# Performance work log

Measured on AMD Instinct MI355X. Metric: run time of the kernel, lower is better.

Reference implementation:

```python
import jax, jax.numpy as jnp
import numpy as np

TEMPERATURE = 0.07
NEG_INF = -9e15
EPS = 1e-12

def setup_inputs() -> dict:
    key = jax.random.key(0)
    k1, k2 = jax.random.split(key)
    N, D = 8192, 128
    features = jax.random.normal(k1, (N, D), dtype=jnp.float32)
    labels = jax.random.randint(k2, (N,), 0, 16, dtype=jnp.int64)
    return {"features": features, "labels": labels}

def reference(features, labels):
    N = features.shape[0]
    # L2 normalize rows (torch F.normalize: x / max(||x||, eps))
    norm = jnp.linalg.norm(features, axis=1, keepdims=True)
    f = features / jnp.maximum(norm, EPS)
    # [N, N] similarity
    sim = jnp.matmul(f, f.T) / TEMPERATURE
    eye = jnp.eye(N, dtype=bool)
    sim = jnp.where(eye, NEG_INF, sim)
    # positive-pair mask: same label, excluding self
    pos_mask = ((labels[:, None] == labels[None, :]) & ~eye).astype(sim.dtype)
    denom = jnp.exp(sim).sum(axis=1, keepdims=True)  # [N, 1]
    log_prob = sim - jnp.log(denom + EPS)
    loss = -(pos_mask * log_prob).sum(axis=1) / (pos_mask.sum(axis=1) + EPS)
    return loss.mean()
```

## Files before the change

### kernel.cpp

```cpp
#include <hip/hip_runtime.h>
#include <hip/hip_bf16.h>

#define EPS 1e-12f
#define SQRT_C_EXP 4.53981597f
#define M_LN2F 0.69314718056f
#define NUM_CLASSES 16
#define CS_BLOCKS 128

#define BM 256
#define BN 128
#define KD 128
#define NCHUNK 8
#define NPART 16

typedef __attribute__((ext_vector_type(4))) float f32x4;
typedef __attribute__((ext_vector_type(8))) short bf16x8;

__device__ __forceinline__ float bf2f(ushort u) {
    unsigned int x = ((unsigned int)u) << 16;
    return __uint_as_float(x);
}

__device__ __forceinline__ const bf16x8* lds_frag(const ushort* base, int r, int slot) {
    int sw = slot ^ (r & 7);
    return reinterpret_cast<const bf16x8*>(
        reinterpret_cast<const char*>(base) + r * 256 + sw * 16);
}

__global__ void normalize_kernel(const float* __restrict__ feat,
                                 ushort* __restrict__ fb,
                                 float* __restrict__ sq,
                                 float* __restrict__ gz,
                                 int N) {
    if (blockIdx.x == 0) {
        for (int i = threadIdx.x; i < NUM_CLASSES * KD + NUM_CLASSES; i += 256)
            gz[i] = 0.f;
    }
    int r    = (blockIdx.x * blockDim.x + threadIdx.x) >> 6;
    int lane = threadIdx.x & 63;
    if (r >= N) return;
    const float2 v = *reinterpret_cast<const float2*>(feat + (size_t)r * KD + lane * 2);
    float s = v.x * v.x + v.y * v.y;
    #pragma unroll
    for (int off = 1; off < 64; off <<= 1) s += __shfl_xor(s, off);
    const float scale = SQRT_C_EXP / fmaxf(sqrtf(s), EPS);

    __hip_bfloat16 h0 = __float2bfloat16(v.x * scale);
    __hip_bfloat16 h1 = __float2bfloat16(v.y * scale);
    ushort u0 = *reinterpret_cast<ushort*>(&h0);
    ushort u1 = *reinterpret_cast<ushort*>(&h1);
    unsigned int pack = (unsigned int)u0 | ((unsigned int)u1 << 16);
    *reinterpret_cast<unsigned int*>(fb + (size_t)r * KD + lane * 2) = pack;

    float q0 = bf2f(u0), q1 = bf2f(u1);
    float q = q0 * q0 + q1 * q1;
    #pragma unroll
    for (int off = 1; off < 64; off <<= 1) q += __shfl_xor(q, off);
    if (lane == 0) sq[r] = q;
}

__global__ __launch_bounds__(256) void classsum_kernel(
    const ushort* __restrict__ fb,
    const int* __restrict__ labels,
    float* __restrict__ g,
    float* __restrict__ cntf,
    int N) {
    __shared__ float lds[2][NUM_CLASSES][128];
    __shared__ float ldc[2][NUM_CLASSES];
    const int d    = threadIdx.x & 127;
    const int half = threadIdx.x >> 7;
    #pragma unroll
    for (int c = 0; c < NUM_CLASSES; c++) lds[half][c][d] = 0.f;
    if (d < NUM_CLASSES) ldc[half][d] = 0.f;
    __syncthreads();

    const int r0 = blockIdx.x * 64 + half * 32;
    for (int r = r0; r < r0 + 32; r++) {
        int lab = labels[r];
        lds[half][lab][d] += bf2f(fb[(size_t)r * KD + d]);
        if (d == 0) ldc[half][lab] += 1.f;
    }
    __syncthreads();

    for (int c = half; c < NUM_CLASSES; c += 2)
        atomicAdd(&g[c * KD + d], lds[0][c][d] + lds[1][c][d]);
    if (threadIdx.x < NUM_CLASSES)
        atomicAdd(&cntf[threadIdx.x], ldc[0][threadIdx.x] + ldc[1][threadIdx.x]);
}

__global__ __launch_bounds__(512, 2) void supcon_denom(
    const ushort* __restrict__ fb,
    float* __restrict__ denom_part,
    int N) {

    __shared__ __align__(16) ushort As[BM * KD];
    __shared__ __align__(16) ushort Bs[2][BN * KD];

    const int tid  = threadIdx.x;
    const int lane = tid & 63;
    const int w    = tid >> 6;
    const int wr   = w >> 1;
    const int wc   = w & 1;
    const int r16  = lane & 15;
    const int g4   = lane >> 4;

    const int rowbase = blockIdx.y * BM;
    const int col0    = blockIdx.x * (BN * NCHUNK);

    {
        const ushort* gA = fb + (size_t)rowbase * KD;
        #pragma unroll
        for (int i = 0; i < 8; i++) {
            int c = i * 512 + tid;
            bf16x8 v = *reinterpret_cast<const bf16x8*>(gA + c * 8);
            int dst = c ^ ((c >> 4) & 7);
            *reinterpret_cast<bf16x8*>(&As[dst * 8]) = v;
        }
        const ushort* gB = fb + (size_t)col0 * KD;
        #pragma unroll
        for (int i = 0; i < 4; i++) {
            int c = i * 512 + tid;
            bf16x8 v = *reinterpret_cast<const bf16x8*>(gB + c * 8);
            int dst = c ^ ((c >> 4) & 7);
            *reinterpret_cast<bf16x8*>(&Bs[0][dst * 8]) = v;
        }
    }
    __syncthreads();

    bf16x8 a[4][4];
    #pragma unroll
    for (int ks = 0; ks < 4; ks++) {
        const int slot = ks * 4 + g4;
        #pragma unroll
        for (int m = 0; m < 4; m++)
            a[ks][m] = *lds_frag(As, wr * 64 + m * 16 + r16, slot);
    }

    float pd[4][4];
    #pragma unroll
    for (int m = 0; m < 4; m++)
        #pragma unroll
        for (int i = 0; i < 4; i++) pd[m][i] = 0.f;

    int cur = 0;
    for (int c = 0; c < NCHUNK; c++) {
        bf16x8 pre0, pre1, pre2, pre3;
        if (c + 1 < NCHUNK) {
            const ushort* gB = fb + (size_t)(col0 + (c + 1) * BN) * KD;
            pre0 = *reinterpret_cast<const bf16x8*>(gB + (0 * 512 + tid) * 8);
            pre1 = *reinterpret_cast<const bf16x8*>(gB + (1 * 512 + tid) * 8);
            pre2 = *reinterpret_cast<const bf16x8*>(gB + (2 * 512 + tid) * 8);
            pre3 = *reinterpret_cast<const bf16x8*>(gB + (3 * 512 + tid) * 8);
        }

        f32x4 acc[4][4];
        #pragma unroll
        for (int m = 0; m < 4; m++)
            #pragma unroll
            for (int n = 0; n < 4; n++) acc[m][n] = f32x4{0.f, 0.f, 0.f, 0.f};

        const ushort* bbase = Bs[cur];
        #pragma unroll
        for (int ks = 0; ks < 4; ks++) {
            const int slot = ks * 4 + g4;
            bf16x8 bv[4];
            #pragma unroll
            for (int n = 0; n < 4; n++)
                bv[n] = *lds_frag(bbase, wc * 64 + n * 16 + r16, slot);
            #pragma unroll
            for (int m = 0; m < 4; m++)
                #pragma unroll
                for (int n = 0; n < 4; n++)
                    acc[m][n] = __builtin_amdgcn_mfma_f32_16x16x32_bf16(a[ks][m], bv[n], acc[m][n], 0, 0, 0);
        }

        #pragma unroll
        for (int m = 0; m < 4; m++)
            #pragma unroll
            for (int n = 0; n < 4; n++)
                #pragma unroll
                for (int i = 0; i < 4; i++)
                    pd[m][i] += __builtin_amdgcn_exp2f(acc[m][n][i]);

        if (c + 1 < NCHUNK) {
            ushort* dstb = Bs[cur ^ 1];
            int ch;
            ch = 0 * 512 + tid; *reinterpret_cast<bf16x8*>(&dstb[(ch ^ ((ch >> 4) & 7)) * 8]) = pre0;
            ch = 1 * 512 + tid; *reinterpret_cast<bf16x8*>(&dstb[(ch ^ ((ch >> 4) & 7)) * 8]) = pre1;
            ch = 2 * 512 + tid; *reinterpret_cast<bf16x8*>(&dstb[(ch ^ ((ch >> 4) & 7)) * 8]) = pre2;
            ch = 3 * 512 + tid; *reinterpret_cast<bf16x8*>(&dstb[(ch ^ ((ch >> 4) & 7)) * 8]) = pre3;
        }
        __syncthreads();
        cur ^= 1;
    }

    #pragma unroll
    for (int off = 1; off < 16; off <<= 1)
        #pragma unroll
        for (int m = 0; m < 4; m++)
            #pragma unroll
            for (int i = 0; i < 4; i++)
                pd[m][i] += __shfl_xor(pd[m][i], off);

    if (r16 == 0) {
        const int part = blockIdx.x * 2 + wc;
        #pragma unroll
        for (int m = 0; m < 4; m++)
            #pragma unroll
            for (int i = 0; i < 4; i++) {
                int r = rowbase + wr * 64 + m * 16 + g4 * 4 + i;
                denom_part[(size_t)r * NPART + part] = pd[m][i];
            }
    }
}

__global__ void rowloss_kernel(const ushort* __restrict__ fb,
                               const int* __restrict__ labels,
                               const float* __restrict__ denom_part,
                               const float* __restrict__ sq,
                               const float* __restrict__ g,
                               const float* __restrict__ cntf,
                               float* __restrict__ rowloss,
                               int N) {
    int r    = (blockIdx.x * blockDim.x + threadIdx.x) >> 6;
    int lane = threadIdx.x & 63;
    if (r >= N) return;
    int lab = labels[r];
    unsigned int pk = *reinterpret_cast<const unsigned int*>(fb + (size_t)r * KD + lane * 2);
    float f0 = bf2f((ushort)(pk & 0xffff));
    float f1 = bf2f((ushort)(pk >> 16));
    const float2 gv = *reinterpret_cast<const float2*>(g + lab * KD + lane * 2);
    float p = f0 * gv.x + f1 * gv.y;
    #pragma unroll
    for (int off = 1; off < 64; off <<= 1) p += __shfl_xor(p, off);

    float dsum = (lane < NPART) ? denom_part[(size_t)r * NPART + lane] : 0.f;
    #pragma unroll
    for (int off = 1; off < NPART; off <<= 1) dsum += __shfl_xor(dsum, off);

    if (lane == 0) {
        float sqr    = sq[r];
        float possum = (p - sqr) * M_LN2F;
        float cnt    = cntf[lab] - 1.0f;
        float dn     = dsum - __builtin_amdgcn_exp2f(sqr);
        rowloss[r]   = -(possum - cnt * logf(dn + EPS)) / (cnt + EPS);
    }
}

__global__ void reduce_kernel(const float* __restrict__ rowloss,
                              float* __restrict__ out, int N) {
    __shared__ float sdata[16];
    float s = 0.f;
    for (int r = threadIdx.x; r < N; r += blockDim.x) s += rowloss[r];
    #pragma unroll
    for (int off = 1; off < 64; off <<= 1) s += __shfl_xor(s, off);
    int wv = threadIdx.x >> 6;
    if ((threadIdx.x & 63) == 0) sdata[wv] = s;
    __syncthreads();
    if (threadIdx.x == 0) {
        float t = 0.f;
        int nw = (int)(blockDim.x >> 6);
        for (int i = 0; i < nw; i++) t += sdata[i];
        out[0] = t / (float)N;
    }
}

extern "C" void kernel_launch(void* const* d_in, const int* in_sizes, int n_in,
                              void* d_out, int out_size, void* d_ws, size_t ws_size,
                              hipStream_t stream) {
    const float* feat = (const float*)d_in[0];
    const int* labels = (const int*)d_in[1];
    const int N = in_sizes[1];

    char* ws = (char*)d_ws;
    size_t off = 0;
    ushort* fb = (ushort*)(ws + off);                 off += (size_t)N * KD * sizeof(ushort);
    float* g     = (float*)(ws + off);                off += (size_t)NUM_CLASSES * KD * sizeof(float);
    float* cntf  = (float*)(ws + off);                off += (size_t)NUM_CLASSES * sizeof(float);
    float* sq         = (float*)(ws + off);           off += (size_t)N * sizeof(float);
    float* denom_part = (float*)(ws + off);           off += (size_t)N * NPART * sizeof(float);
    float* rowloss    = (float*)(ws + off);

    normalize_kernel<<<(N + 3) / 4, 256, 0, stream>>>(feat, fb, sq, g, N);
    classsum_kernel<<<CS_BLOCKS, 256, 0, stream>>>(fb, labels, g, cntf, N);

    dim3 grid(N / (BN * NCHUNK), N / BM);
    supcon_denom<<<grid, 512, 0, stream>>>(fb, denom_part, N);

    rowloss_kernel<<<(N + 3) / 4, 256, 0, stream>>>(fb, labels, denom_part, sq, g, cntf, rowloss, N);
    reduce_kernel<<<1, 1024, 0, stream>>>(rowloss, (float*)d_out, N);
}
```

Before: 50.29 us.

## Shrink denom tiles and stream B chunks directly into LDS via global_load_lds

The similarity-denominator kernel's tiles shrink from 256x128 to 128x64, with 8 column groups of 16 chunks each, so twice as many partials per row are written. Global-to-LDS copies now use the global_load_lds builtin with the swizzle applied on the source address, so data no longer passes through registers. Each wave now holds a 4x1 MFMA accumulator tile instead of 4x4, and launch bounds rise to 4 blocks per CU for higher occupancy. In exchange each B fragment is reused across fewer MFMAs, per-block arithmetic intensity drops, and there are more chunk syncs per unit of work.

```diff
diff --git a/kernel.cpp b/kernel.cpp
--- a/kernel.cpp
+++ b/kernel.cpp
@@ -7,11 +7,12 @@
 #define NUM_CLASSES 16
 #define CS_BLOCKS 128
 
-#define BM 256
-#define BN 128
+#define BM 128
+#define BN 64
 #define KD 128
-#define NCHUNK 8
-#define NPART 16
+#define NCHUNK 16
+#define NCOLG 8
+#define NPART 32
 
 typedef __attribute__((ext_vector_type(4))) float f32x4;
 typedef __attribute__((ext_vector_type(8))) short bf16x8;
@@ -19,6 +20,12 @@
 __device__ __forceinline__ float bf2f(ushort u) {
     unsigned int x = ((unsigned int)u) << 16;
     return __uint_as_float(x);
+}
+
+__device__ __forceinline__ void gload16(const void* g, void* l) {
+    __builtin_amdgcn_global_load_lds(
+        (const __attribute__((address_space(1))) void*)g,
+        (__attribute__((address_space(3))) void*)l, 16, 0, 0);
 }
 
 __device__ __forceinline__ const bf16x8* lds_frag(const ushort* base, int r, int slot) {
@@ -88,7 +95,7 @@
         atomicAdd(&cntf[threadIdx.x], ldc[0][threadIdx.x] + ldc[1][threadIdx.x]);
 }
 
-__global__ __launch_bounds__(512, 2) void supcon_denom(
+__global__ __launch_bounds__(512, 4) void supcon_denom(
     const ushort* __restrict__ fb,
     float* __restrict__ denom_part,
     int N) {
@@ -99,8 +106,8 @@
     const int tid  = threadIdx.x;
     const int lane = tid & 63;
     const int w    = tid >> 6;
-    const int wr   = w >> 1;
-    const int wc   = w & 1;
+    const int wr   = w >> 2;
+    const int wc   = w & 3;
     const int r16  = lane & 15;
     const int g4   = lane >> 4;
 
@@ -110,19 +117,17 @@
     {
         const ushort* gA = fb + (size_t)rowbase * KD;
         #pragma unroll
-        for (int i = 0; i < 8; i++) {
-            int c = i * 512 + tid;
-            bf16x8 v = *reinterpret_cast<const bf16x8*>(gA + c * 8);
-            int dst = c ^ ((c >> 4) & 7);
-            *reinterpret_cast<bf16x8*>(&As[dst * 8]) = v;
+        for (int i = 0; i < 4; i++) {
+            int d = i * 512 + tid;
+            int s = d ^ ((d >> 4) & 7);
+            gload16(gA + (size_t)s * 8, &As[d * 8]);
         }
         const ushort* gB = fb + (size_t)col0 * KD;
         #pragma unroll
-        for (int i = 0; i < 4; i++) {
-            int c = i * 512 + tid;
-            bf16x8 v = *reinterpret_cast<const bf16x8*>(gB + c * 8);
-            int dst = c ^ ((c >> 4) & 7);
-            *reinterpret_cast<bf16x8*>(&Bs[0][dst * 8]) = v;
+        for (int i = 0; i < 2; i++) {
+            int d = i * 512 + tid;
+            int s = d ^ ((d >> 4) & 7);
+            gload16(gB + (size_t)s * 8, &Bs[0][d * 8]);
         }
     }
     __syncthreads();
@@ -144,52 +149,37 @@
 
     int cur = 0;
     for (int c = 0; c < NCHUNK; c++) {
-        bf16x8 pre0, pre1, pre2, pre3;
         if (c + 1 < NCHUNK) {
             const ushort* gB = fb + (size_t)(col0 + (c + 1) * BN) * KD;
-            pre0 = *reinterpret_cast<const bf16x8*>(gB + (0 * 512 + tid) * 8);
-            pre1 = *reinterpret_cast<const bf16x8*>(gB + (1 * 512 + tid) * 8);
-            pre2 = *reinterpret_cast<const bf16x8*>(gB + (2 * 512 + tid) * 8);
-            pre3 = *reinterpret_cast<const bf16x8*>(gB + (3 * 512 + tid) * 8);
-        }
-
-        f32x4 acc[4][4];
-        #pragma unroll
-        for (int m = 0; m < 4; m++)
-            #pragma unroll
-            for (int n = 0; n < 4; n++) acc[m][n] = f32x4{0.f, 0.f, 0.f, 0.f};
+            ushort* dstb = Bs[cur ^ 1];
+            #pragma unroll
+            for (int i = 0; i < 2; i++) {
+                int d = i * 512 + tid;
+                int s = d ^ ((d >> 4) & 7);
+                gload16(gB + (size_t)s * 8, &dstb[d * 8]);
+            }
+        }
+
+        f32x4 acc[4];
+        #pragma unroll
+        for (int m = 0; m < 4; m++) acc[m] = f32x4{0.f, 0.f, 0.f, 0.f};
 
         const ushort* bbase = Bs[cur];
         #pragma unroll
         for (int ks = 0; ks < 4; ks++) {
             const int slot = ks * 4 + g4;
-            bf16x8 bv[4];
-            #pragma unroll
-            for (int n = 0; n < 4; n++)
-                bv[n] = *lds_frag(bbase, wc * 64 + n * 16 + r16, slot);
+            bf16x8 bv = *lds_frag(bbase, wc * 16 + r16, slot);
             #pragma unroll
             for (int m = 0; m < 4; m++)
-                #pragma unroll
-                for (int n = 0; n < 4; n++)
-                    acc[m][n] = __builtin_amdgcn_mfma_f32_16x16x32_bf16(a[ks][m], bv[n], acc[m][n], 0, 0, 0);
-        }
-
-        #pragma unroll
-        for (int m = 0; m < 4; m++)
-            #pragma unroll
-            for (int n = 0; n < 4; n++)
-                #pragma unroll
-                for (int i = 0; i < 4; i++)
-                    pd[m][i] += __builtin_amdgcn_exp2f(acc[m][n][i]);
-
-        if (c + 1 < NCHUNK) {
-            ushort* dstb = Bs[cur ^ 1];
-            int ch;
-            ch = 0 * 512 + tid; *reinterpret_cast<bf16x8*>(&dstb[(ch ^ ((ch >> 4) & 7)) * 8]) = pre0;
-            ch = 1 * 512 + tid; *reinterpret_cast<bf16x8*>(&dstb[(ch ^ ((ch >> 4) & 7)) * 8]) = pre1;
-            ch = 2 * 512 + tid; *reinterpret_cast<bf16x8*>(&dstb[(ch ^ ((ch >> 4) & 7)) * 8]) = pre2;
-            ch = 3 * 512 + tid; *reinterpret_cast<bf16x8*>(&dstb[(ch ^ ((ch >> 4) & 7)) * 8]) = pre3;
-        }
+                acc[m] = __builtin_amdgcn_mfma_f32_16x16x32_bf16(a[ks][m], bv, acc[m], 0, 0, 0);
+        }
+
+        #pragma unroll
+        for (int m = 0; m < 4; m++)
+            #pragma unroll
+            for (int i = 0; i < 4; i++)
+                pd[m][i] += __builtin_amdgcn_exp2f(acc[m][i]);
+
         __syncthreads();
         cur ^= 1;
     }
@@ -203,7 +193,7 @@
                 pd[m][i] += __shfl_xor(pd[m][i], off);
 
     if (r16 == 0) {
-        const int part = blockIdx.x * 2 + wc;
+        const int part = blockIdx.x * 4 + wc;
         #pragma unroll
         for (int m = 0; m < 4; m++)
             #pragma unroll
@@ -284,7 +274,7 @@
     normalize_kernel<<<(N + 3) / 4, 256, 0, stream>>>(feat, fb, sq, g, N);
     classsum_kernel<<<CS_BLOCKS, 256, 0, stream>>>(fb, labels, g, cntf, N);
 
-    dim3 grid(N / (BN * NCHUNK), N / BM);
+    dim3 grid(NCOLG, N / BM);
     supcon_denom<<<grid, 512, 0, stream>>>(fb, denom_part, N);
 
     rowloss_kernel<<<(N + 3) / 4, 256, 0, stream>>>(fb, labels, denom_part, sq, g, cntf, rowloss, N);
```

After: 50.66 us. Within noise of the previous version (+0.7%).

## Fuse positive-pair sums into the GEMM epilogue and drop class-sum kernel

Applied to the files above, without the earlier changes.

Removes the separate class-sum kernel, which used atomics, and the zeroing of its buffer. Instead, the similarity GEMM kernel loads row and column labels and accumulates the positive-pair similarity sum and count per row next to the exp denominator. The row-loss kernel then only reduces the 48 partials per row. This saves one launch and the class-sum pass, but adds label loads, compare/select work and extra registers and shuffles inside the hot GEMM loop, which could lower occupancy.

```diff
diff --git a/kernel.cpp b/kernel.cpp
--- a/kernel.cpp
+++ b/kernel.cpp
@@ -5,13 +5,13 @@
 #define SQRT_C_EXP 4.53981597f
 #define M_LN2F 0.69314718056f
 #define NUM_CLASSES 16
-#define CS_BLOCKS 128
 
 #define BM 256
 #define BN 128
 #define KD 128
 #define NCHUNK 8
 #define NPART 16
+#define PSTRIDE 48
 
 typedef __attribute__((ext_vector_type(4))) float f32x4;
 typedef __attribute__((ext_vector_type(8))) short bf16x8;
@@ -30,12 +30,7 @@
 __global__ void normalize_kernel(const float* __restrict__ feat,
                                  ushort* __restrict__ fb,
                                  float* __restrict__ sq,
-                                 float* __restrict__ gz,
                                  int N) {
-    if (blockIdx.x == 0) {
-        for (int i = threadIdx.x; i < NUM_CLASSES * KD + NUM_CLASSES; i += 256)
-            gz[i] = 0.f;
-    }
     int r    = (blockIdx.x * blockDim.x + threadIdx.x) >> 6;
     int lane = threadIdx.x & 63;
     if (r >= N) return;
@@ -59,38 +54,10 @@
     if (lane == 0) sq[r] = q;
 }
 
-__global__ __launch_bounds__(256) void classsum_kernel(
+__global__ __launch_bounds__(512, 2) void supcon_denom(
     const ushort* __restrict__ fb,
     const int* __restrict__ labels,
-    float* __restrict__ g,
-    float* __restrict__ cntf,
-    int N) {
-    __shared__ float lds[2][NUM_CLASSES][128];
-    __shared__ float ldc[2][NUM_CLASSES];
-    const int d    = threadIdx.x & 127;
-    const int half = threadIdx.x >> 7;
-    #pragma unroll
-    for (int c = 0; c < NUM_CLASSES; c++) lds[half][c][d] = 0.f;
-    if (d < NUM_CLASSES) ldc[half][d] = 0.f;
-    __syncthreads();
-
-    const int r0 = blockIdx.x * 64 + half * 32;
-    for (int r = r0; r < r0 + 32; r++) {
-        int lab = labels[r];
-        lds[half][lab][d] += bf2f(fb[(size_t)r * KD + d]);
-        if (d == 0) ldc[half][lab] += 1.f;
-    }
-    __syncthreads();
-
-    for (int c = half; c < NUM_CLASSES; c += 2)
-        atomicAdd(&g[c * KD + d], lds[0][c][d] + lds[1][c][d]);
-    if (threadIdx.x < NUM_CLASSES)
-        atomicAdd(&cntf[threadIdx.x], ldc[0][threadIdx.x] + ldc[1][threadIdx.x]);
-}
-
-__global__ __launch_bounds__(512, 2) void supcon_denom(
-    const ushort* __restrict__ fb,
-    float* __restrict__ denom_part,
+    float* __restrict__ part,
     int N) {
 
     __shared__ __align__(16) ushort As[BM * KD];
@@ -125,6 +92,14 @@
             *reinterpret_cast<bf16x8*>(&Bs[0][dst * 8]) = v;
         }
     }
+
+    int rlab[4][4];
+    #pragma unroll
+    for (int m = 0; m < 4; m++)
+        #pragma unroll
+        for (int i = 0; i < 4; i++)
+            rlab[m][i] = labels[rowbase + wr * 64 + m * 16 + g4 * 4 + i];
+
     __syncthreads();
 
     bf16x8 a[4][4];
@@ -136,11 +111,11 @@
             a[ks][m] = *lds_frag(As, wr * 64 + m * 16 + r16, slot);
     }
 
-    float pd[4][4];
+    float pd[4][4], pp[4][4], pc[4][4];
     #pragma unroll
     for (int m = 0; m < 4; m++)
         #pragma unroll
-        for (int i = 0; i < 4; i++) pd[m][i] = 0.f;
+        for (int i = 0; i < 4; i++) { pd[m][i] = 0.f; pp[m][i] = 0.f; pc[m][i] = 0.f; }
 
     int cur = 0;
     for (int c = 0; c < NCHUNK; c++) {
@@ -152,6 +127,11 @@
             pre2 = *reinterpret_cast<const bf16x8*>(gB + (2 * 512 + tid) * 8);
             pre3 = *reinterpret_cast<const bf16x8*>(gB + (3 * 512 + tid) * 8);
         }
+        const int colbase = col0 + c * BN + wc * 64;
+        int clab[4];
+        #pragma unroll
+        for (int n = 0; n < 4; n++)
+            clab[n] = labels[colbase + n * 16 + r16];
 
         f32x4 acc[4][4];
         #pragma unroll
@@ -179,8 +159,13 @@
             #pragma unroll
             for (int n = 0; n < 4; n++)
                 #pragma unroll
-                for (int i = 0; i < 4; i++)
-                    pd[m][i] += __builtin_amdgcn_exp2f(acc[m][n][i]);
+                for (int i = 0; i < 4; i++) {
+                    const float sim = acc[m][n][i];
+                    pd[m][i] += __builtin_amdgcn_exp2f(sim);
+                    const bool mt = (rlab[m][i] == clab[n]);
+                    pp[m][i] += mt ? sim : 0.f;
+                    pc[m][i] += mt ? 1.f : 0.f;
+                }
 
         if (c + 1 < NCHUNK) {
             ushort* dstb = Bs[cur ^ 1];
@@ -199,49 +184,46 @@
         #pragma unroll
         for (int m = 0; m < 4; m++)
             #pragma unroll
-            for (int i = 0; i < 4; i++)
+            for (int i = 0; i < 4; i++) {
                 pd[m][i] += __shfl_xor(pd[m][i], off);
+                pp[m][i] += __shfl_xor(pp[m][i], off);
+                pc[m][i] += __shfl_xor(pc[m][i], off);
+            }
 
     if (r16 == 0) {
-        const int part = blockIdx.x * 2 + wc;
+        const int slot = blockIdx.x * 2 + wc;
         #pragma unroll
         for (int m = 0; m < 4; m++)
             #pragma unroll
             for (int i = 0; i < 4; i++) {
                 int r = rowbase + wr * 64 + m * 16 + g4 * 4 + i;
-                denom_part[(size_t)r * NPART + part] = pd[m][i];
+                float* p = part + (size_t)r * PSTRIDE + slot;
+                p[0]  = pd[m][i];
+                p[16] = pp[m][i];
+                p[32] = pc[m][i];
             }
     }
 }
 
-__global__ void rowloss_kernel(const ushort* __restrict__ fb,
-                               const int* __restrict__ labels,
-                               const float* __restrict__ denom_part,
+__global__ void rowloss_kernel(const float* __restrict__ part,
                                const float* __restrict__ sq,
-                               const float* __restrict__ g,
-                               const float* __restrict__ cntf,
                                float* __restrict__ rowloss,
                                int N) {
     int r    = (blockIdx.x * blockDim.x + threadIdx.x) >> 6;
     int lane = threadIdx.x & 63;
     if (r >= N) return;
-    int lab = labels[r];
-    unsigned int pk = *reinterpret_cast<const unsigned int*>(fb + (size_t)r * KD + lane * 2);
-    float f0 = bf2f((ushort)(pk & 0xffff));
-    float f1 = bf2f((ushort)(pk >> 16));
-    const float2 gv = *reinterpret_cast<const float2*>(g + lab * KD + lane * 2);
-    float p = f0 * gv.x + f1 * gv.y;
-    #pragma unroll
-    for (int off = 1; off < 64; off <<= 1) p += __shfl_xor(p, off);
-
-    float dsum = (lane < NPART) ? denom_part[(size_t)r * NPART + lane] : 0.f;
-    #pragma unroll
-    for (int off = 1; off < NPART; off <<= 1) dsum += __shfl_xor(dsum, off);
+
+    float v = (lane < PSTRIDE) ? part[(size_t)r * PSTRIDE + lane] : 0.f;
+    #pragma unroll
+    for (int off = 1; off < 16; off <<= 1) v += __shfl_xor(v, off);
+    float dsum = __shfl(v, 0);
+    float psum = __shfl(v, 16);
+    float csum = __shfl(v, 32);
 
     if (lane == 0) {
         float sqr    = sq[r];
-        float possum = (p - sqr) * M_LN2F;
-        float cnt    = cntf[lab] - 1.0f;
+        float possum = (psum - sqr) * M_LN2F;
+        float cnt    = csum - 1.0f;
         float dn     = dsum - __builtin_amdgcn_exp2f(sqr);
         rowloss[r]   = -(possum - cnt * logf(dn + EPS)) / (cnt + EPS);
     }
@@ -274,19 +256,16 @@
 
     char* ws = (char*)d_ws;
     size_t off = 0;
-    ushort* fb = (ushort*)(ws + off);                 off += (size_t)N * KD * sizeof(ushort);
-    float* g     = (float*)(ws + off);                off += (size_t)NUM_CLASSES * KD * sizeof(float);
-    float* cntf  = (float*)(ws + off);                off += (size_t)NUM_CLASSES * sizeof(float);
-    float* sq         = (float*)(ws + off);           off += (size_t)N * sizeof(float);
-    float* denom_part = (float*)(ws + off);           off += (size_t)N * NPART * sizeof(float);
-    float* rowloss    = (float*)(ws + off);
-
-    normalize_kernel<<<(N + 3) / 4, 256, 0, stream>>>(feat, fb, sq, g, N);
-    classsum_kernel<<<CS_BLOCKS, 256, 0, stream>>>(fb, labels, g, cntf, N);
+    ushort* fb     = (ushort*)(ws + off);  off += (size_t)N * KD * sizeof(ushort);
+    float* sq      = (float*)(ws + off);   off += (size_t)N * sizeof(float);
+    float* part    = (float*)(ws + off);   off += (size_t)N * PSTRIDE * sizeof(float);
+    float* rowloss = (float*)(ws + off);
+
+    normalize_kernel<<<(N + 3) / 4, 256, 0, stream>>>(feat, fb, sq, N);
 
     dim3 grid(N / (BN * NCHUNK), N / BM);
-    supcon_denom<<<grid, 512, 0, stream>>>(fb, denom_part, N);
-
-    rowloss_kernel<<<(N + 3) / 4, 256, 0, stream>>>(fb, labels, denom_part, sq, g, cntf, rowloss, N);
+    supcon_denom<<<grid, 512, 0, stream>>>(fb, labels, part, N);
+
+    rowloss_kernel<<<(N + 3) / 4, 256, 0, stream>>>(part, sq, rowloss, N);
     reduce_kernel<<<1, 1024, 0, stream>>>(rowloss, (float*)d_out, N);
 }
```

New measurement: 48.74 us. 3.1% less time.
